# Performance work log

Hardware: AMD Instinct MI355X
Metric: run time of the kernel (lower is better)

The kernel has to match this reference:

```python
import jax, jax.numpy as jnp
import numpy as np

N = 100000
E = 1600000
D = 128  # out_dim == head_dim (num_heads = 1)


def setup_inputs() -> dict:
    key = jax.random.key(0)
    ks = jax.random.split(key, 16)
    s = 0.05
    inp = {
        "h": jax.random.normal(ks[0], (N, D), dtype=jnp.float32),
        "c": jax.random.normal(ks[1], (N, 3), dtype=jnp.float32),
        "src": jax.random.randint(ks[2], (E,), 0, N),
        "dst": jax.random.randint(ks[3], (E,), 0, N),
        # Q/K/V projections (use_bias=False)
        "Wq": jax.random.normal(ks[4], (D, D), dtype=jnp.float32) * s,
        "Wk": jax.random.normal(ks[5], (D, D), dtype=jnp.float32) * s,
        "Wv": jax.random.normal(ks[6], (D, D), dtype=jnp.float32) * s,
        # linear_p: Linear(3,3) -> ReLU -> Linear(3,D)
        "Wp1": jax.random.normal(ks[7], (3, 3), dtype=jnp.float32) * s,
        "bp1": jnp.zeros((3,), dtype=jnp.float32),
        "Wp2": jax.random.normal(ks[8], (3, D), dtype=jnp.float32) * s,
        "bp2": jnp.zeros((D,), dtype=jnp.float32),
        # edge MLP: Linear(D,D) -> ReLU -> Linear(D,1)
        "We1": jax.random.normal(ks[9], (D, D), dtype=jnp.float32) * s,
        "be1": jnp.zeros((D,), dtype=jnp.float32),
        "We2": jax.random.normal(ks[10], (D, 1), dtype=jnp.float32) * s,
        "be2": jnp.zeros((1,), dtype=jnp.float32),
        # output projection O (has bias)
        "Wo": jax.random.normal(ks[11], (D, D), dtype=jnp.float32) * s,
        "bo": jnp.zeros((D,), dtype=jnp.float32),
    }
    return inp


def reference(h, c, src, dst, Wq, Wk, Wv, Wp1, bp1, Wp2, bp2,
              We1, be1, We2, be2, Wo, bo):
    scale = np.sqrt(np.float32(D))  # sqrt(out_dim) used by scaled_exp
    n = h.shape[0]
    # node projections
    Q = h @ Wq                                   # [N, D]
    K = h @ Wk                                   # [N, D]
    V = h @ Wv                                   # [N, D]
    P = jax.nn.relu(c @ Wp1 + bp1) @ Wp2 + bp2   # [N, D] position encoding
    # per-edge point-transformer score: MLP(K[src] - Q[dst] + P[src])
    dif = K[src] - Q[dst] + P[src]               # [E, D]
    raw = jax.nn.relu(dif @ We1 + be1) @ We2 + be2  # [E, 1]
    score = jnp.exp(jnp.clip(raw / scale, -5.0, 5.0))  # [E, 1]
    # gather-multiply-scatter: weighted V+P sum and normalizer z per dst node
    msg = (V + P)[src] * score                   # [E, D]
    wV = jax.ops.segment_sum(msg, dst, num_segments=n)    # [N, D]
    z = jax.ops.segment_sum(score, dst, num_segments=n)   # [N, 1]
    head_out = wV / z                            # [N, D]
    return head_out @ Wo + bo                    # [N, D]
```

## Files before the change

kernel.cpp:

```cpp
#include <hip/hip_runtime.h>
#include <math.h>

#define DD 128
#define CAP 10240
typedef unsigned int u32;
typedef unsigned short u16;
typedef __attribute__((ext_vector_type(8))) short bf16x8;
typedef __attribute__((ext_vector_type(4))) float f32x4;
typedef __attribute__((ext_vector_type(2))) float f32x2;

__device__ __forceinline__ float4 f4zero() { return make_float4(0.f, 0.f, 0.f, 0.f); }
__device__ __forceinline__ u32 bf16rne(float f) {
    u32 u = __float_as_uint(f);
    u += 0x7FFFu + ((u >> 16) & 1u);
    return u >> 16;
}
__device__ __forceinline__ u32 pack2(float lo, float hi) {
    return bf16rne(lo) | (bf16rne(hi) << 16);
}
__device__ __forceinline__ float unlo(u32 u) { return __uint_as_float(u << 16); }
__device__ __forceinline__ float unhi(u32 u) { return __uint_as_float(u & 0xFFFF0000u); }

__global__ __launch_bounds__(256) void fused_pre(
    const float* __restrict__ Wq, const float* __restrict__ Wk,
    const float* __restrict__ Wv, const float* __restrict__ We1,
    const float* __restrict__ be1, const float* __restrict__ Wp2,
    const float* __restrict__ bp2, const float* __restrict__ Wo,
    u32* __restrict__ BF,
    const int* __restrict__ src, const int* __restrict__ dst,
    int* __restrict__ gcount, u32* __restrict__ ebuf, int E) {
    const int t = threadIdx.x;
    if (blockIdx.x < 38) {
        const int bid = blockIdx.x * 4 + (t >> 6);
        const int l = t & 63;
        const int c = l & 15;
        const int kg = l >> 4;
        float val[8];

        if (bid < 120) {
            const int ct = bid / 5, ks = bid - ct * 5;
            const int u = ct / 6, r = ct - u * 6;
            const int n = 32 * u + 16 * (r < 2 ? r : (r & 1)) + c;
#pragma unroll
            for (int j = 0; j < 8; ++j) {
                const int k = ks * 32 + kg * 8 + j;
                float v = 0.f;
                if (r < 2) {
                    if (k < 128) {
                        float a = 0.f;
                        for (int q = 0; q < 128; ++q)
                            a = fmaf(Wq[k * 128 + q], We1[q * 128 + n], a);
                        v = a;
                    }
                } else if (r < 4) {
                    if (k < 128) {
                        float a = 0.f;
                        for (int q = 0; q < 128; ++q)
                            a = fmaf(Wk[k * 128 + q], We1[q * 128 + n], a);
                        v = a;
                    } else if (k < 131) {
                        float a = 0.f;
                        for (int q = 0; q < 128; ++q)
                            a = fmaf(Wp2[(k - 128) * 128 + q], We1[q * 128 + n], a);
                        v = a;
                    } else if (k == 131) {
                        float a = be1[n];
                        for (int q = 0; q < 128; ++q)
                            a = fmaf(bp2[q], We1[q * 128 + n], a);
                        v = a;
                    }
                } else {
                    if (k < 128) v = Wv[k * 128 + n];
                    else if (k < 131) v = Wp2[(k - 128) * 128 + n];
                    else if (k == 131) v = bp2[n];
                }
                val[j] = v;
            }
        } else {
            const int b2 = bid - 120;
            const int ct = b2 >> 2, ks = b2 & 3;
            const int n = ct * 16 + c;
#pragma unroll
            for (int j = 0; j < 8; ++j) {
                const int k = ks * 32 + kg * 8 + j;
                val[j] = Wo[k * 128 + n];
            }
        }
        u32* dp = &BF[((size_t)bid * 64 + l) * 4];
        dp[0] = pack2(val[0], val[1]);
        dp[1] = pack2(val[2], val[3]);
        dp[2] = pack2(val[4], val[5]);
        dp[3] = pack2(val[6], val[7]);
    } else {
        __shared__ int hist[256];
        __shared__ int base[256];
        hist[t] = 0;
        __syncthreads();
        const int chunk = (blockIdx.x - 38) * 4096;
        int bk[16], rk[16];
        u32 pv[16];
#pragma unroll
        for (int i = 0; i < 16; ++i) {
            int idx = chunk + i * 256 + t;
            bk[i] = -1;
            if (idx < E) {
                int dd = dst[idx];
                int ss = src[idx];
                bk[i] = dd >> 9;
                pv[i] = ((u32)ss << 9) | (u32)(dd & 511);
                rk[i] = atomicAdd(&hist[bk[i]], 1);
            }
        }
        __syncthreads();
        if (hist[t]) base[t] = t * CAP + atomicAdd(&gcount[t], hist[t]);
        __syncthreads();
#pragma unroll
        for (int i = 0; i < 16; ++i) {
            if (bk[i] >= 0) ebuf[base[bk[i]] + rk[i]] = pv[i];
        }
    }
}

__global__ __launch_bounds__(256) void scanB_we2r(
    const int* __restrict__ gcount, int* __restrict__ bucket_base,
    const float* __restrict__ We2, float* __restrict__ We2r) {
    __shared__ int s[256];
    int t = threadIdx.x;
    int orig = gcount[t];
    s[t] = orig;
    __syncthreads();
    for (int off = 1; off < 256; off <<= 1) {
        int x = (t >= off) ? s[t - off] : 0;
        __syncthreads();
        s[t] += x;
        __syncthreads();
    }
    bucket_base[t] = s[t] - orig;
    if (t < 128) {
        int col = 32 * (t >> 5) + 16 * (t & 1) + ((t & 31) >> 1);
        We2r[t] = We2[col];
    }
}

__global__ __launch_bounds__(256) void fused_mid(
    const float* __restrict__ h, const float* __restrict__ c,
    const float* __restrict__ Wp1, const float* __restrict__ bp1,
    const u32* __restrict__ BF,
    u32* __restrict__ QWb, unsigned char* __restrict__ KV, int N,
    const int* __restrict__ gcount, const int* __restrict__ bucket_base,
    const u32* __restrict__ ebuf, int* __restrict__ ssrc,
    int* __restrict__ offs, int E, int NR) {
    __shared__ u32 lds[64 * 96];
    const int t = threadIdx.x;

    if ((int)blockIdx.x < NR) {
        int* cnt = (int*)lds;
        int* cur = cnt + 512;
        int* ts = cur + 512;
        const int r = blockIdx.x;
        const int cnt_r = gcount[r];
        const int base_r = bucket_base[r];
        cnt[t] = 0;
        cnt[t + 256] = 0;
        __syncthreads();
        const u32* eb = &ebuf[(size_t)r * CAP];
        for (int i = t; i < cnt_r; i += 256) atomicAdd(&cnt[eb[i] & 511], 1);
        __syncthreads();
        int v0 = cnt[2 * t], v1 = cnt[2 * t + 1];
        int pair = v0 + v1;
        ts[t] = pair;
        __syncthreads();
        for (int off = 1; off < 256; off <<= 1) {
            int x = (t >= off) ? ts[t - off] : 0;
            __syncthreads();
            ts[t] += x;
            __syncthreads();
        }
        int ex = ts[t] - pair;
        cur[2 * t] = ex;
        cur[2 * t + 1] = ex + v0;
        offs[r * 512 + 2 * t] = base_r + ex;
        offs[r * 512 + 2 * t + 1] = base_r + ex + v0;
        if (r == NR - 1 && t == 255) offs[NR * 512] = E;
        __syncthreads();
        for (int i = t; i < cnt_r; i += 256) {
            u32 e = eb[i];
            int p = atomicAdd(&cur[e & 511], 1);
            ssrc[base_r + p] = (int)(e >> 9);
        }
    } else {
        u32* hs = lds;
        const int row0 = ((int)blockIdx.x - NR) * 64;

#pragma unroll
        for (int i = 0; i < 8; ++i) {
            int f = t + i * 256;
            int row = f >> 5;
            int cq = f & 31;
            float4 v = f4zero();
            if (row0 + row < N) v = *(const float4*)&h[(size_t)(row0 + row) * DD + cq * 4];
            int idx = row * 96 + ((cq * 2) ^ ((row & 7) << 2));
            uint2 p;
            p.x = pack2(v.x, v.y);
            p.y = pack2(v.z, v.w);
            *(uint2*)&hs[idx] = p;
        }
        if (t < 64) {
            int row = t;
            float u0 = 0.f, u1 = 0.f, u2 = 0.f;
            if (row0 + row < N) {
                const float* cr = &c[(size_t)(row0 + row) * 3];
                float c0 = cr[0], c1 = cr[1], c2 = cr[2];
                u0 = fmaxf(bp1[0] + c0 * Wp1[0] + c1 * Wp1[3] + c2 * Wp1[6], 0.f);
                u1 = fmaxf(bp1[1] + c0 * Wp1[1] + c1 * Wp1[4] + c2 * Wp1[7], 0.f);
                u2 = fmaxf(bp1[2] + c0 * Wp1[2] + c1 * Wp1[5] + c2 * Wp1[8], 0.f);
            }
            int swz = (row & 7) << 2;
            uint4 z0 = make_uint4(pack2(u0, u1), pack2(u2, 1.0f), 0u, 0u);
            uint4 zz = make_uint4(0u, 0u, 0u, 0u);
#pragma unroll
            for (int q = 0; q < 4; ++q) {
                int idx = row * 96 + 64 + ((q * 4) ^ swz);
                *(uint4*)&hs[idx] = (q == 0) ? z0 : zz;
            }
        }
        __syncthreads();

        const int w = t >> 6, l = t & 63;
        const int cc = l & 15, kg = l >> 4;

        f32x4 acc[4][6];
#pragma unroll
        for (int rt = 0; rt < 4; ++rt)
#pragma unroll
            for (int r = 0; r < 6; ++r) acc[rt][r] = (f32x4){0.f, 0.f, 0.f, 0.f};

#pragma unroll
        for (int ks = 0; ks < 5; ++ks) {
            bf16x8 a[4];
#pragma unroll
            for (int rt = 0; rt < 4; ++rt) {
                int row = rt * 16 + cc;
                int idx = row * 96 + ((ks * 16 + kg * 4) ^ ((row & 7) << 2));
                a[rt] = *(const bf16x8*)&hs[idx];
            }
#pragma unroll
            for (int r = 0; r < 6; ++r) {
                const bf16x8 b = *(const bf16x8*)&BF[(((size_t)(w * 6 + r) * 5 + ks) * 64 + l) * 4];
#pragma unroll
                for (int rt = 0; rt < 4; ++rt)
                    acc[rt][r] = __builtin_amdgcn_mfma_f32_16x16x32_bf16(a[rt], b, acc[rt][r], 0, 0, 0);
            }
        }

#pragma unroll
        for (int rt = 0; rt < 4; ++rt) {
#pragma unroll
            for (int j = 0; j < 4; ++j) {
                int row = row0 + rt * 16 + kg * 4 + j;
                if (row >= N) continue;
                QWb[(size_t)row * 64 + w * 16 + cc] = pack2(acc[rt][0][j], acc[rt][1][j]);
                unsigned char* kvrow = &KV[(size_t)row * 384];
                u32 kp = __builtin_amdgcn_cvt_pk_fp8_f32(acc[rt][2][j], acc[rt][3][j], 0u, false);
                *(u16*)&kvrow[w * 32 + cc * 2] = (u16)kp;
                *(u32*)&kvrow[128 + 4 * (w * 16 + cc)] = pack2(acc[rt][4][j], acc[rt][5][j]);
            }
        }
    }
}

__global__ __launch_bounds__(256) void aggregate(
    const int* __restrict__ offs, const int* __restrict__ ssrc,
    const unsigned char* __restrict__ KV, const u32* __restrict__ QWb,
    const float* __restrict__ We2r, const float* __restrict__ be2,
    u32* __restrict__ headb, int N) {
    const int node = (blockIdx.x * 256 + threadIdx.x) >> 6;
    const int lane = threadIdx.x & 63;
    if (node >= N) return;
    const int g = lane >> 4, i = lane & 15;

    const float SC = 0.08838834764831845f * 1.4426950408889634f;
    const float CL = 5.0f * 1.4426950408889634f;

    uint4 Qu = *(const uint4*)&QWb[(size_t)node * 64 + 4 * i];
    f32x2 q01 = {unlo(Qu.x), unhi(Qu.x)};
    f32x2 q23 = {unlo(Qu.y), unhi(Qu.y)};
    f32x2 q45 = {unlo(Qu.z), unhi(Qu.z)};
    f32x2 q67 = {unlo(Qu.w), unhi(Qu.w)};
    f32x2 w01 = *(const f32x2*)&We2r[8 * i];
    f32x2 w23 = *(const f32x2*)&We2r[8 * i + 2];
    f32x2 w45 = *(const f32x2*)&We2r[8 * i + 4];
    f32x2 w67 = *(const f32x2*)&We2r[8 * i + 6];
    const float B2SC = be2[0] * SC;
    const f32x2 zero2 = {0.f, 0.f};

    const int beg = offs[node], end = offs[node + 1];
    f32x2 acc01 = zero2, acc23 = zero2, acc45 = zero2, acc67 = zero2;
    float zacc = 0.f;

    int e = beg + g;
    int s = (e < end) ? ssrc[e] : 0;
    for (int e0 = beg; e0 < end; e0 += 4) {
        const bool act = (e0 + g) < end;
        const unsigned char* row = &KV[(size_t)s * 384];
        uint2 kk = *(const uint2*)&row[8 * i];
        uint4 vv = *(const uint4*)&row[128 + 16 * i];
        int en = e0 + 4 + g;
        s = (en < end) ? ssrc[en] : 0;

        f32x2 d, p2;
        d = __builtin_amdgcn_cvt_pk_f32_fp8(kk.x, false) - q01;
        d = __builtin_elementwise_max(d, zero2);
        p2 = d * w01;
        d = __builtin_amdgcn_cvt_pk_f32_fp8(kk.x, true) - q23;
        d = __builtin_elementwise_max(d, zero2);
        p2 += d * w23;
        d = __builtin_amdgcn_cvt_pk_f32_fp8(kk.y, false) - q45;
        d = __builtin_elementwise_max(d, zero2);
        p2 += d * w45;
        d = __builtin_amdgcn_cvt_pk_f32_fp8(kk.y, true) - q67;
        d = __builtin_elementwise_max(d, zero2);
        p2 += d * w67;
        float p = p2[0] + p2[1];
#pragma unroll
        for (int off = 1; off <= 8; off <<= 1) p += __shfl_xor(p, off);

        float targ = fmaf(p, SC, B2SC);
        targ = fminf(fmaxf(targ, -CL), CL);
        float sc = act ? exp2f(targ) : 0.f;
        f32x2 sc2 = {sc, sc};

        f32x2 v;
        v = (f32x2){unlo(vv.x), unhi(vv.x)}; acc01 += v * sc2;
        v = (f32x2){unlo(vv.y), unhi(vv.y)}; acc23 += v * sc2;
        v = (f32x2){unlo(vv.z), unhi(vv.z)}; acc45 += v * sc2;
        v = (f32x2){unlo(vv.w), unhi(vv.w)}; acc67 += v * sc2;
        zacc += sc;
    }

    float a0 = acc01[0], a1 = acc01[1], a2 = acc23[0], a3 = acc23[1];
    float a4 = acc45[0], a5 = acc45[1], a6 = acc67[0], a7 = acc67[1];

    a0 += __shfl_xor(a0, 16); a0 += __shfl_xor(a0, 32);
    a1 += __shfl_xor(a1, 16); a1 += __shfl_xor(a1, 32);
    a2 += __shfl_xor(a2, 16); a2 += __shfl_xor(a2, 32);
    a3 += __shfl_xor(a3, 16); a3 += __shfl_xor(a3, 32);
    a4 += __shfl_xor(a4, 16); a4 += __shfl_xor(a4, 32);
    a5 += __shfl_xor(a5, 16); a5 += __shfl_xor(a5, 32);
    a6 += __shfl_xor(a6, 16); a6 += __shfl_xor(a6, 32);
    a7 += __shfl_xor(a7, 16); a7 += __shfl_xor(a7, 32);
    zacc += __shfl_xor(zacc, 16); zacc += __shfl_xor(zacc, 32);

    if (g == 0) {
        float rz = 1.0f / zacc;
        uint4 o;
        o.x = pack2(a0 * rz, a1 * rz);
        o.y = pack2(a2 * rz, a3 * rz);
        o.z = pack2(a4 * rz, a5 * rz);
        o.w = pack2(a6 * rz, a7 * rz);
        *(uint4*)&headb[(size_t)node * 64 + 4 * i] = o;
    }
}

__global__ __launch_bounds__(256) void out_mfma(
    const u32* __restrict__ headb, const u32* __restrict__ WoF,
    const float* __restrict__ bo, float* __restrict__ out, int N) {
    __shared__ u32 hs[64 * 64];

    const int row0 = blockIdx.x * 64;
    const int t = threadIdx.x;

#pragma unroll
    for (int i = 0; i < 4; ++i) {
        int f = t + i * 256;
        int row = f >> 4;
        int cq = f & 15;
        uint4 v = make_uint4(0u, 0u, 0u, 0u);
        if (row0 + row < N) v = *(const uint4*)&headb[(size_t)(row0 + row) * 64 + cq * 4];
        int m = cq >> 2;
        int cb = (cq & 3) * 4;
        int swz = (row & 7) << 2;
        uint2 A, B;
        A.x = (v.x & 0xFFFFu) | (v.y << 16);
        A.y = (v.z & 0xFFFFu) | (v.w << 16);
        B.x = (v.x >> 16) | (v.y & 0xFFFF0000u);
        B.y = (v.z >> 16) | (v.w & 0xFFFF0000u);
        int dA = 16 * m + (cb >> 1);
        *(uint2*)&hs[row * 64 + (dA ^ swz)] = A;
        *(uint2*)&hs[row * 64 + ((dA + 8) ^ swz)] = B;
    }
    __syncthreads();

    const int w = t >> 6, l = t & 63;
    const int cc = l & 15, kg = l >> 4;

    f32x4 acc[4][2];
#pragma unroll
    for (int rt = 0; rt < 4; ++rt) {
        acc[rt][0] = (f32x4){0.f, 0.f, 0.f, 0.f};
        acc[rt][1] = (f32x4){0.f, 0.f, 0.f, 0.f};
    }

#pragma unroll
    for (int ks = 0; ks < 4; ++ks) {
        bf16x8 a[4];
#pragma unroll
        for (int rt = 0; rt < 4; ++rt) {
            int row = rt * 16 + cc;
            int idx = row * 64 + ((ks * 16 + kg * 4) ^ ((row & 7) << 2));
            a[rt] = *(const bf16x8*)&hs[idx];
        }
#pragma unroll
        for (int ctl = 0; ctl < 2; ++ctl) {
            const bf16x8 b = *(const bf16x8*)&WoF[(((size_t)(2 * w + ctl) * 4 + ks) * 64 + l) * 4];
#pragma unroll
            for (int rt = 0; rt < 4; ++rt)
                acc[rt][ctl] = __builtin_amdgcn_mfma_f32_16x16x32_bf16(a[rt], b, acc[rt][ctl], 0, 0, 0);
        }
    }

#pragma unroll
    for (int ctl = 0; ctl < 2; ++ctl) {
        int col = (2 * w + ctl) * 16 + cc;
        float bias = bo[col];
#pragma unroll
        for (int rt = 0; rt < 4; ++rt) {
#pragma unroll
            for (int j = 0; j < 4; ++j) {
                int row = row0 + rt * 16 + kg * 4 + j;
                if (row >= N) continue;
                out[(size_t)row * DD + col] = acc[rt][ctl][j] + bias;
            }
        }
    }
}

extern "C" void kernel_launch(void* const* d_in, const int* in_sizes, int n_in,
                              void* d_out, int out_size, void* d_ws, size_t ws_size,
                              hipStream_t stream) {
    const float* h   = (const float*)d_in[0];
    const float* c   = (const float*)d_in[1];
    const int*   src = (const int*)d_in[2];
    const int*   dst = (const int*)d_in[3];
    const float* Wq  = (const float*)d_in[4];
    const float* Wk  = (const float*)d_in[5];
    const float* Wv  = (const float*)d_in[6];
    const float* Wp1 = (const float*)d_in[7];
    const float* bp1 = (const float*)d_in[8];
    const float* Wp2 = (const float*)d_in[9];
    const float* bp2 = (const float*)d_in[10];
    const float* We1 = (const float*)d_in[11];
    const float* be1 = (const float*)d_in[12];
    const float* We2 = (const float*)d_in[13];
    const float* be2 = (const float*)d_in[14];
    const float* Wo  = (const float*)d_in[15];
    const float* bo  = (const float*)d_in[16];

    const int N = in_sizes[0] / DD;
    const int E = in_sizes[2];
    const int NR = (N + 511) >> 9;
    const int NB1 = (E + 4095) / 4096;
    const int NG = (N + 63) / 64;

    u32* BF    = (u32*)d_ws;
    u32* WoF   = BF + 120 * 256;
    u32* QWb   = BF + 152 * 256;
    unsigned char* KV = (unsigned char*)(QWb + (size_t)N * 64);
    u32* headb = (u32*)(KV + (size_t)N * 384);
    int* offs  = (int*)(headb + (size_t)N * 64);
    int* gcount = offs + ((size_t)NR * 512 + 1);
    int* bbase  = gcount + 256;
    float* We2r = (float*)(bbase + 256);
    int* ssrc   = (int*)(We2r + 128);
    u32* ebuf   = (u32*)(ssrc + E);

    hipMemsetAsync(gcount, 0, 256 * sizeof(int), stream);

    fused_pre<<<38 + NB1, 256, 0, stream>>>(Wq, Wk, Wv, We1, be1, Wp2, bp2, Wo,
                                            BF, src, dst, gcount, ebuf, E);

    scanB_we2r<<<1, 256, 0, stream>>>(gcount, bbase, We2, We2r);

    fused_mid<<<NR + NG, 256, 0, stream>>>(
        h, c, Wp1, bp1, BF, QWb, KV, N,
        gcount, bbase, ebuf, ssrc, offs, E, NR);

    aggregate<<<(N * 64 + 255) / 256, 256, 0, stream>>>(offs, ssrc, KV, QWb,
                                                        We2r, be2, headb, N);

    out_mfma<<<NG, 256, 0, stream>>>(headb, WoF, bo, (float*)d_out, N);
}
```

Baseline: 211.2 us.

## Fold output projection Wo into V weights and drop the final GEMM kernel

Uses linearity (sum of score*(V+P))/z @ Wo = sum of score*((V+P)@Wo)/z to precompute Wv@Wo, Wp2@Wo and bp2@Wo in the weight-prep kernel. The V slice of the node projection therefore already lives in output space, and aggregate writes fp32 output plus bias directly. This removes the out_mfma kernel, the headb round trip through memory and one launch. The folded weights are rounded to bf16 after the product, which changes rounding behaviour slightly.

```diff
diff --git a/kernel.cpp b/kernel.cpp
--- a/kernel.cpp
+++ b/kernel.cpp
@@ -30,61 +30,63 @@
     const int* __restrict__ src, const int* __restrict__ dst,
     int* __restrict__ gcount, u32* __restrict__ ebuf, int E) {
     const int t = threadIdx.x;
-    if (blockIdx.x < 38) {
+    if (blockIdx.x < 30) {
         const int bid = blockIdx.x * 4 + (t >> 6);
         const int l = t & 63;
         const int c = l & 15;
         const int kg = l >> 4;
         float val[8];
 
-        if (bid < 120) {
-            const int ct = bid / 5, ks = bid - ct * 5;
-            const int u = ct / 6, r = ct - u * 6;
-            const int n = 32 * u + 16 * (r < 2 ? r : (r & 1)) + c;
-#pragma unroll
-            for (int j = 0; j < 8; ++j) {
-                const int k = ks * 32 + kg * 8 + j;
-                float v = 0.f;
-                if (r < 2) {
-                    if (k < 128) {
-                        float a = 0.f;
-                        for (int q = 0; q < 128; ++q)
-                            a = fmaf(Wq[k * 128 + q], We1[q * 128 + n], a);
-                        v = a;
-                    }
-                } else if (r < 4) {
-                    if (k < 128) {
-                        float a = 0.f;
-                        for (int q = 0; q < 128; ++q)
-                            a = fmaf(Wk[k * 128 + q], We1[q * 128 + n], a);
-                        v = a;
-                    } else if (k < 131) {
-                        float a = 0.f;
-                        for (int q = 0; q < 128; ++q)
-                            a = fmaf(Wp2[(k - 128) * 128 + q], We1[q * 128 + n], a);
-                        v = a;
-                    } else if (k == 131) {
-                        float a = be1[n];
-                        for (int q = 0; q < 128; ++q)
-                            a = fmaf(bp2[q], We1[q * 128 + n], a);
-                        v = a;
-                    }
-                } else {
-                    if (k < 128) v = Wv[k * 128 + n];
-                    else if (k < 131) v = Wp2[(k - 128) * 128 + n];
-                    else if (k == 131) v = bp2[n];
+        const int ct = bid / 5, ks = bid - ct * 5;
+        const int u = ct / 6, r = ct - u * 6;
+        const int n = 32 * u + 16 * (r < 2 ? r : (r & 1)) + c;
+#pragma unroll
+        for (int j = 0; j < 8; ++j) {
+            const int k = ks * 32 + kg * 8 + j;
+            float v = 0.f;
+            if (r < 2) {
+                if (k < 128) {
+                    float a = 0.f;
+                    for (int q = 0; q < 128; ++q)
+                        a = fmaf(Wq[k * 128 + q], We1[q * 128 + n], a);
+                    v = a;
                 }
-                val[j] = v;
-            }
-        } else {
-            const int b2 = bid - 120;
-            const int ct = b2 >> 2, ks = b2 & 3;
-            const int n = ct * 16 + c;
-#pragma unroll
-            for (int j = 0; j < 8; ++j) {
-                const int k = ks * 32 + kg * 8 + j;
-                val[j] = Wo[k * 128 + n];
-            }
+            } else if (r < 4) {
+                if (k < 128) {
+                    float a = 0.f;
+                    for (int q = 0; q < 128; ++q)
+                        a = fmaf(Wk[k * 128 + q], We1[q * 128 + n], a);
+                    v = a;
+                } else if (k < 131) {
+                    float a = 0.f;
+                    for (int q = 0; q < 128; ++q)
+                        a = fmaf(Wp2[(k - 128) * 128 + q], We1[q * 128 + n], a);
+                    v = a;
+                } else if (k == 131) {
+                    float a = be1[n];
+                    for (int q = 0; q < 128; ++q)
+                        a = fmaf(bp2[q], We1[q * 128 + n], a);
+                    v = a;
+                }
+            } else {
+                if (k < 128) {
+                    float a = 0.f;
+                    for (int q = 0; q < 128; ++q)
+                        a = fmaf(Wv[k * 128 + q], Wo[q * 128 + n], a);
+                    v = a;
+                } else if (k < 131) {
+                    float a = 0.f;
+                    for (int q = 0; q < 128; ++q)
+                        a = fmaf(Wp2[(k - 128) * 128 + q], Wo[q * 128 + n], a);
+                    v = a;
+                } else if (k == 131) {
+                    float a = 0.f;
+                    for (int q = 0; q < 128; ++q)
+                        a = fmaf(bp2[q], Wo[q * 128 + n], a);
+                    v = a;
+                }
+            }
+            val[j] = v;
         }
         u32* dp = &BF[((size_t)bid * 64 + l) * 4];
         dp[0] = pack2(val[0], val[1]);
@@ -96,7 +98,7 @@
         __shared__ int base[256];
         hist[t] = 0;
         __syncthreads();
-        const int chunk = (blockIdx.x - 38) * 4096;
+        const int chunk = (blockIdx.x - 30) * 4096;
         int bk[16], rk[16];
         u32 pv[16];
 #pragma unroll
@@ -273,7 +275,7 @@
     const int* __restrict__ offs, const int* __restrict__ ssrc,
     const unsigned char* __restrict__ KV, const u32* __restrict__ QWb,
     const float* __restrict__ We2r, const float* __restrict__ be2,
-    u32* __restrict__ headb, int N) {
+    const float* __restrict__ bo, float* __restrict__ out, int N) {
     const int node = (blockIdx.x * 256 + threadIdx.x) >> 6;
     const int lane = threadIdx.x & 63;
     if (node >= N) return;
@@ -353,85 +355,16 @@
 
     if (g == 0) {
         float rz = 1.0f / zacc;
-        uint4 o;
-        o.x = pack2(a0 * rz, a1 * rz);
-        o.y = pack2(a2 * rz, a3 * rz);
-        o.z = pack2(a4 * rz, a5 * rz);
-        o.w = pack2(a6 * rz, a7 * rz);
-        *(uint4*)&headb[(size_t)node * 64 + 4 * i] = o;
-    }
-}
-
-__global__ __launch_bounds__(256) void out_mfma(
-    const u32* __restrict__ headb, const u32* __restrict__ WoF,
-    const float* __restrict__ bo, float* __restrict__ out, int N) {
-    __shared__ u32 hs[64 * 64];
-
-    const int row0 = blockIdx.x * 64;
-    const int t = threadIdx.x;
-
-#pragma unroll
-    for (int i = 0; i < 4; ++i) {
-        int f = t + i * 256;
-        int row = f >> 4;
-        int cq = f & 15;
-        uint4 v = make_uint4(0u, 0u, 0u, 0u);
-        if (row0 + row < N) v = *(const uint4*)&headb[(size_t)(row0 + row) * 64 + cq * 4];
-        int m = cq >> 2;
-        int cb = (cq & 3) * 4;
-        int swz = (row & 7) << 2;
-        uint2 A, B;
-        A.x = (v.x & 0xFFFFu) | (v.y << 16);
-        A.y = (v.z & 0xFFFFu) | (v.w << 16);
-        B.x = (v.x >> 16) | (v.y & 0xFFFF0000u);
-        B.y = (v.z >> 16) | (v.w & 0xFFFF0000u);
-        int dA = 16 * m + (cb >> 1);
-        *(uint2*)&hs[row * 64 + (dA ^ swz)] = A;
-        *(uint2*)&hs[row * 64 + ((dA + 8) ^ swz)] = B;
-    }
-    __syncthreads();
-
-    const int w = t >> 6, l = t & 63;
-    const int cc = l & 15, kg = l >> 4;
-
-    f32x4 acc[4][2];
-#pragma unroll
-    for (int rt = 0; rt < 4; ++rt) {
-        acc[rt][0] = (f32x4){0.f, 0.f, 0.f, 0.f};
-        acc[rt][1] = (f32x4){0.f, 0.f, 0.f, 0.f};
-    }
-
-#pragma unroll
-    for (int ks = 0; ks < 4; ++ks) {
-        bf16x8 a[4];
-#pragma unroll
-        for (int rt = 0; rt < 4; ++rt) {
-            int row = rt * 16 + cc;
-            int idx = row * 64 + ((ks * 16 + kg * 4) ^ ((row & 7) << 2));
-            a[rt] = *(const bf16x8*)&hs[idx];
-        }
-#pragma unroll
-        for (int ctl = 0; ctl < 2; ++ctl) {
-            const bf16x8 b = *(const bf16x8*)&WoF[(((size_t)(2 * w + ctl) * 4 + ks) * 64 + l) * 4];
-#pragma unroll
-            for (int rt = 0; rt < 4; ++rt)
-                acc[rt][ctl] = __builtin_amdgcn_mfma_f32_16x16x32_bf16(a[rt], b, acc[rt][ctl], 0, 0, 0);
-        }
-    }
-
-#pragma unroll
-    for (int ctl = 0; ctl < 2; ++ctl) {
-        int col = (2 * w + ctl) * 16 + cc;
-        float bias = bo[col];
-#pragma unroll
-        for (int rt = 0; rt < 4; ++rt) {
-#pragma unroll
-            for (int j = 0; j < 4; ++j) {
-                int row = row0 + rt * 16 + kg * 4 + j;
-                if (row >= N) continue;
-                out[(size_t)row * DD + col] = acc[rt][ctl][j] + bias;
-            }
-        }
+        const int base = 32 * (i >> 2) + 4 * (i & 3);
+        float4 bA = *(const float4*)&bo[base];
+        float4 bB = *(const float4*)&bo[base + 16];
+        float4 oA = make_float4(fmaf(a0, rz, bA.x), fmaf(a2, rz, bA.y),
+                                fmaf(a4, rz, bA.z), fmaf(a6, rz, bA.w));
+        float4 oB = make_float4(fmaf(a1, rz, bB.x), fmaf(a3, rz, bB.y),
+                                fmaf(a5, rz, bB.z), fmaf(a7, rz, bB.w));
+        float* orow = &out[(size_t)node * DD];
+        *(float4*)&orow[base] = oA;
+        *(float4*)&orow[base + 16] = oB;
     }
 }
 
@@ -463,11 +396,9 @@
     const int NG = (N + 63) / 64;
 
     u32* BF    = (u32*)d_ws;
-    u32* WoF   = BF + 120 * 256;
-    u32* QWb   = BF + 152 * 256;
+    u32* QWb   = BF + 120 * 256;
     unsigned char* KV = (unsigned char*)(QWb + (size_t)N * 64);
-    u32* headb = (u32*)(KV + (size_t)N * 384);
-    int* offs  = (int*)(headb + (size_t)N * 64);
+    int* offs  = (int*)(KV + (size_t)N * 384);
     int* gcount = offs + ((size_t)NR * 512 + 1);
     int* bbase  = gcount + 256;
     float* We2r = (float*)(bbase + 256);
@@ -476,7 +407,7 @@
 
     hipMemsetAsync(gcount, 0, 256 * sizeof(int), stream);
 
-    fused_pre<<<38 + NB1, 256, 0, stream>>>(Wq, Wk, Wv, We1, be1, Wp2, bp2, Wo,
+    fused_pre<<<30 + NB1, 256, 0, stream>>>(Wq, Wk, Wv, We1, be1, Wp2, bp2, Wo,
                                             BF, src, dst, gcount, ebuf, E);
 
     scanB_we2r<<<1, 256, 0, stream>>>(gcount, bbase, We2, We2r);
@@ -485,8 +416,6 @@
         h, c, Wp1, bp1, BF, QWb, KV, N,
         gcount, bbase, ebuf, ssrc, offs, E, NR);
 
-    aggregate<<<(N * 64 + 255) / 256, 256, 0, stream>>>(offs, ssrc, KV, QWb,
-                                                        We2r, be2, headb, N);
-
-    out_mfma<<<NG, 256, 0, stream>>>(headb, WoF, bo, (float*)d_out, N);
-}
+    aggregate<<<(N * 64 + 255) / 256, 256, 0, stream>>>(
+        offs, ssrc, KV, QWb, We2r, be2, bo, (float*)d_out, N);
+}
```

After: 195.8 us. -7.3%, faster.
